# Performance work log

Hardware: AMD Instinct MI355X
Metric: run time of the kernel (lower is better)

## Reference

```python
import jax, jax.numpy as jnp
import numpy as np

PS = 3        # patch_size
RATE = 2      # rate
FS = 3        # fuse_kernel_size
SS = 10.0     # softmax_scale
PAD = (PS - 1) // 2       # tl.calc_padding(ps, 1)
FUSE_PAD = (FS - 1) // 2  # tl.calc_padding(fs, 1)
EPS = 1e-4


def extract_patches(x, ps, stride, pad):
    """x: (B,C,H,W) -> (B, L, C, ps, ps); L row-major over output positions (== F.unfold order)."""
    B, C, H, W = x.shape
    xp = jnp.pad(x, ((0, 0), (0, 0), (pad, pad), (pad, pad)))
    oh = (H + 2 * pad - ps) // stride + 1
    ow = (W + 2 * pad - ps) // stride + 1
    rows = []
    for dy in range(ps):  # small fixed loop (ps=3)
        cols = []
        for dx in range(ps):
            cols.append(xp[:, :, dy:dy + (oh - 1) * stride + 1:stride,
                              dx:dx + (ow - 1) * stride + 1:stride])
        rows.append(jnp.stack(cols, axis=2))           # (B,C,ps,oh,ow)
    p = jnp.stack(rows, axis=2)                        # (B,C,ps,ps,oh,ow)
    return p.reshape(B, C, ps, ps, oh * ow).transpose(0, 4, 1, 2, 3)


def diag_fuse(S, fs, pad):
    """conv2d of (N,N) 'image' with identity fs x fs kernel (diagonal smoothing)."""
    N = S.shape[0]
    Sp = jnp.pad(S, ((pad, pad), (pad, pad)))
    out = Sp[0:N, 0:N]
    for k in range(1, fs):  # fs=3, tiny fixed loop
        out = out + Sp[k:k + N, k:k + N]
    return out


def fuse_scores(S, hr, wr):
    L = hr * wr
    S = diag_fuse(S, FS, FUSE_PAD)
    S = S.reshape(hr, wr, hr, wr).transpose(1, 0, 3, 2).reshape(L, L)
    S = diag_fuse(S, FS, FUSE_PAD)
    S = S.reshape(wr, hr, wr, hr).transpose(1, 0, 3, 2).reshape(L, L)
    return S


def contextual_attention(f_o, b_o, mask_o):
    B, c, h, w = f_o.shape
    # nearest downsample by 1/rate == strided slice
    f = f_o[:, :, ::RATE, ::RATE]
    b = b_o[:, :, ::RATE, ::RATE]
    m = mask_o[:, :, ::RATE, ::RATE]
    hr, wr = f.shape[2], f.shape[3]
    L = hr * wr

    fg = extract_patches(f, PS, 1, PAD)        # (B,L,c,ps,ps) foreground neighborhoods
    bs = extract_patches(b, PS, 1, PAD)        # (B,L,c,ps,ps) shrunk bg patches
    bi = extract_patches(b_o, PS, RATE, PAD)   # (B,L,c,ps,ps) full-res bg patches

    bnorm = jnp.maximum(jnp.sqrt(jnp.sum(bs * bs, axis=(2, 3, 4))), EPS)  # (B,L)
    bsn = bs / bnorm[:, :, None, None, None]

    # score[b,p,q] = <normalized bg patch p, fg neighborhood at position q>
    S = jnp.einsum('bpcij,bqcij->bpq', bsn, fg)  # (B,L,L)
    S = jax.vmap(lambda s: fuse_scores(s, hr, wr))(S)

    # valid-patch indicator from downsampled mask
    mp = extract_patches(m, PS, 1, PAD)                                   # (B,L,1,ps,ps)
    valid = (jnp.mean(mp, axis=(2, 3, 4)) == 0.0).astype(f_o.dtype)       # (B,L)

    score = S.reshape(B, L, hr, wr) * valid[:, :, None, None]
    score = jax.nn.softmax(score * SS, axis=1) * valid[:, :, None, None]

    # conv_transpose2d(score, bi, stride=RATE, padding=PAD, output_padding=1) / 4
    wgt = jnp.flip(bi.transpose(0, 2, 1, 3, 4), axis=(-2, -1))  # (B,c,L,ps,ps)
    pad_cfg = [(PS - 1 - PAD, PS - 1 - PAD + 1)] * 2            # output_padding on high side

    def agg(s, wk):  # s:(L,hr,wr), wk:(c,L,ps,ps)
        return jax.lax.conv_general_dilated(
            s[None], wk, (1, 1), pad_cfg, lhs_dilation=(RATE, RATE),
            dimension_numbers=('NCHW', 'OIHW', 'NCHW'))[0]

    out = jax.vmap(agg)(score, wgt) / 4.0   # (B,c,h,w)
    return out


def setup_inputs() -> dict:
    key = jax.random.key(0)
    k1, k2, k3 = jax.random.split(key, 3)
    f_o = jax.random.normal(k1, (16, 128, 64, 64), dtype=jnp.float32)
    b_o = jax.random.normal(k2, (16, 128, 64, 64), dtype=jnp.float32)
    mask_o = jax.random.randint(k3, (16, 1, 64, 64), 0, 2).astype(jnp.float32)
    return {"f_o": f_o, "b_o": b_o, "mask_o": mask_o}


def reference(f_o, b_o, mask_o):
    return contextual_attention(f_o, b_o, mask_o)
```

## Files before the change

kernel.cpp:

```cpp
#include <hip/hip_runtime.h>
#include <cmath>

#define CC 128
#define HH 64
#define WWI 64
#define LL 1024
#define NB 16
#define MM 1152
#define KC 384
#define TPD 1156

#define SLAB      2977808ul
#define OFF_TP    0
#define OFF_S3T   0
#define OFF_W     0
#define OFF_S2    1336336
#define OFF_SCORET 1336336
#define OFF_POOL  2384912
#define OFF_N2    2974736
#define OFF_BNORM 2975760
#define OFF_VALID 2976784

#define NHROW 132
#define NH1 (NHROW * TPD)
#define NHALO (NH1 + 1024 * NHROW)

typedef __bf16 bf16x8 __attribute__((ext_vector_type(8)));
typedef __bf16 bf16x4 __attribute__((ext_vector_type(4)));
typedef float f32x4 __attribute__((ext_vector_type(4)));

#define GLDS(g, l) __builtin_amdgcn_global_load_lds( \
    (const __attribute__((address_space(1))) unsigned int*)(const void*)(g), \
    (__attribute__((address_space(3))) unsigned int*)(void*)(l), 16, 0, 0)

__global__ __launch_bounds__(256) void k_prep(const float* __restrict__ f_o,
                                              const float* __restrict__ b_o,
                                              float* __restrict__ ws,
                                              int b0) {
    int bz = blockIdx.y, gb = b0 + bz;
    int uy = blockIdx.x;
    __shared__ float lf[128 * 33];
    __shared__ float lb[128 * 33];
    __shared__ float red[8 * 32];
    int tid = threadIdx.x;
    int ux = tid & 31, co = tid >> 5;
    size_t pix = (size_t)(2 * uy) * WWI + 2 * ux;
    const float* fbp = f_o + (size_t)gb * CC * HH * WWI + pix;
    const float* bbp = b_o + (size_t)gb * CC * HH * WWI + pix;
#pragma unroll
    for (int pass = 0; pass < 16; pass++) {
        int c = pass * 8 + co;
        lf[c * 33 + ux] = fbp[(size_t)c * HH * WWI];
        lb[c * 33 + ux] = bbp[(size_t)c * HH * WWI];
    }
    __syncthreads();
    int ux2 = tid >> 3, cg = (tid & 7) * 16;
    int u = uy * 32 + ux2;
    __bf16* bcat = (__bf16*)(ws + (size_t)bz * SLAB + OFF_POOL) + (size_t)u * KC;
    __bf16* fcat = bcat + 393216;
    float s2 = 0.f;
#pragma unroll
    for (int k = 0; k < 16; k++) {
        int c = cg + k;
        float fv = lf[c * 33 + ux2];
        float bv = lb[c * 33 + ux2];
        __bf16 fhi = (__bf16)fv; __bf16 flo = (__bf16)(fv - (float)fhi);
        __bf16 bhi = (__bf16)bv; __bf16 blo = (__bf16)(bv - (float)bhi);
        bcat[c] = bhi; bcat[128 + c] = bhi; bcat[256 + c] = blo;
        fcat[c] = fhi; fcat[128 + c] = flo; fcat[256 + c] = fhi;
        s2 += bv * bv;
    }
    red[(tid & 7) * 32 + ux2] = s2;
    __syncthreads();
    if (tid < 32) {
        float s = 0.f;
#pragma unroll
        for (int k = 0; k < 8; k++) s += red[k * 32 + tid];
        ws[(size_t)bz * SLAB + OFF_N2 + uy * 32 + tid] = s;
    }
}

__global__ __launch_bounds__(256) void k_bnorm_valid(float* __restrict__ ws,
                                                     const float* __restrict__ mask,
                                                     int b0) {
    int t = blockIdx.x * 256 + threadIdx.x;
    int p  = t & (LL - 1);
    int bz = t >> 10;
    int gb = b0 + bz;
    int py = p >> 5, px = p & 31;
    const float* mb = mask + (size_t)gb * HH * WWI;
    const float* n2 = ws + (size_t)bz * SLAB + OFF_N2;
    float s = 0.f, msum = 0.f;
#pragma unroll
    for (int dy = -1; dy <= 1; dy++) {
#pragma unroll
        for (int dx = -1; dx <= 1; dx++) {
            int py2 = py + dy, px2 = px + dx;
            if ((unsigned)py2 < 32u && (unsigned)px2 < 32u) {
                s    += n2[(py2 << 5) | px2];
                msum += mb[(2 * py2) * WWI + 2 * px2];
            }
        }
    }
    ws[(size_t)bz * SLAB + OFF_BNORM + p] = fmaxf(sqrtf(s), 1e-4f);
    ws[(size_t)bz * SLAB + OFF_VALID + p] = (msum == 0.0f) ? 1.0f : 0.0f;
}

__device__ __forceinline__ int halo_idx(int k) {
    if (k < 34) return k;
    if (k < 68) return 1122 + (k - 34);
    if (k < 100) return 34 * (k - 100 + 33);
    return 34 * (k - 132 + 33) + 33;
}

__global__ __launch_bounds__(256) void k_zerohalo(float* __restrict__ ws) {
    int bz = blockIdx.y;
    int t = blockIdx.x * 256 + threadIdx.x;
    if (t >= NHALO) return;
    float* Tp = ws + (size_t)bz * SLAB + OFF_TP;
    if (t < NH1) {
        int R = halo_idx(t / TPD);
        Tp[(size_t)R * TPD + (t % TPD)] = 0.f;
    } else {
        int t2 = t - NH1;
        int ir = t2 / NHROW;
        int R  = 34 * (1 + (ir >> 5)) + 1 + (ir & 31);
        int C  = halo_idx(t2 % NHROW);
        Tp[(size_t)R * TPD + C] = 0.f;
    }
}

template<int KTOT>
__device__ __forceinline__ void gemm_core(const __bf16* __restrict__ Ab,
                                          const __bf16* __restrict__ Bb,
                                          int lda, int ldb, int m0, int n0,
                                          __bf16* As, __bf16* Bs,
                                          f32x4 acc[4][4]) {
    int t = threadIdx.x;
    int lane = t & 63, w = t >> 6;
    int rsub = lane >> 3;
    int g8   = ((lane & 7) ^ (rsub & 7)) * 8;
    int lm = lane & 15, kgf = lane >> 4;
    int wm = (w & 1) * 64, wn = (w >> 1) * 64;

#define ISSUE(kt, buf) do {                                                   \
    int k0_ = (kt) * 64;                                                      \
    _Pragma("unroll")                                                         \
    for (int ci = 0; ci < 4; ci++) {                                          \
        int rb = ci * 32 + w * 8;                                             \
        int r  = rb + rsub;                                                   \
        GLDS(Ab + (size_t)(m0 + r) * lda + k0_ + g8, &As[(buf) + rb * 64]);   \
        GLDS(Bb + (size_t)(n0 + r) * ldb + k0_ + g8, &Bs[(buf) + rb * 64]);   \
    } } while (0)

#define COMPUTE(curoff) do {                                                  \
    _Pragma("unroll")                                                         \
    for (int s2 = 0; s2 < 2; s2++) {                                          \
        bf16x8 af[4], bfr[4];                                                 \
        _Pragma("unroll")                                                     \
        for (int i = 0; i < 4; i++)                                           \
            af[i] = *(const bf16x8*)&As[(curoff) + (wm + i * 16 + lm) * 64 +  \
                                        (((s2 * 4 + kgf) ^ (lm & 7)) * 8)];   \
        _Pragma("unroll")                                                     \
        for (int j = 0; j < 4; j++)                                           \
            bfr[j] = *(const bf16x8*)&Bs[(curoff) + (wn + j * 16 + lm) * 64 + \
                                         (((s2 * 4 + kgf) ^ (lm & 7)) * 8)];  \
        _Pragma("unroll")                                                     \
        for (int i = 0; i < 4; i++)                                           \
            _Pragma("unroll")                                                 \
            for (int j = 0; j < 4; j++)                                       \
                acc[i][j] = __builtin_amdgcn_mfma_f32_16x16x32_bf16(          \
                    af[i], bfr[j], acc[i][j], 0, 0, 0);                       \
    } } while (0)

    const int NIT = KTOT / 64;

    ISSUE(0, 0);
    ISSUE(1, 8192);

#pragma unroll 2
    for (int it = 0; it < NIT - 2; it++) {
        int cur = (it & 1) * 8192;
        asm volatile("s_waitcnt vmcnt(8)" ::: "memory");
        __builtin_amdgcn_sched_barrier(0);
        __builtin_amdgcn_s_barrier();
        COMPUTE(cur);
        __builtin_amdgcn_s_barrier();
        ISSUE(it + 2, cur);
    }
    asm volatile("s_waitcnt vmcnt(8)" ::: "memory");
    __builtin_amdgcn_sched_barrier(0);
    __builtin_amdgcn_s_barrier();
    COMPUTE(((NIT - 2) & 1) * 8192);
    __builtin_amdgcn_s_barrier();
    asm volatile("s_waitcnt vmcnt(0)" ::: "memory");
    __builtin_amdgcn_sched_barrier(0);
    __builtin_amdgcn_s_barrier();
    COMPUTE(((NIT - 1) & 1) * 8192);

#undef ISSUE
#undef COMPUTE
}

__global__ __launch_bounds__(256) void k_gemm_T_mfma(float* __restrict__ ws, int swz) {
    int bz, m0, n0;
    if (swz) {
        bz = blockIdx.x + 8 * (blockIdx.z & 1);
        m0 = blockIdx.y * 128;
        n0 = (blockIdx.z >> 1) * 128;
    } else {
        bz = blockIdx.z; m0 = blockIdx.y * 128; n0 = blockIdx.x * 128;
    }
    const __bf16* Ab = (const __bf16*)(ws + (size_t)bz * SLAB + OFF_POOL);
    const __bf16* Bb = Ab + 393216;
    float* Tp = ws + (size_t)bz * SLAB + OFF_TP;
    __shared__ __align__(16) __bf16 As[2 * 128 * 64];
    __shared__ __align__(16) __bf16 Bs[2 * 128 * 64];
    f32x4 acc[4][4];
#pragma unroll
    for (int i = 0; i < 4; i++)
#pragma unroll
        for (int j = 0; j < 4; j++) acc[i][j] = (f32x4)0.0f;
    gemm_core<KC>(Ab, Bb, KC, KC, m0, n0, As, Bs, acc);
    int lane = threadIdx.x & 63, w = threadIdx.x >> 6;
    int lm = lane & 15, kgf = lane >> 4;
    int wm = (w & 1) * 64, wn = (w >> 1) * 64;
#pragma unroll
    for (int i = 0; i < 4; i++) {
#pragma unroll
        for (int r = 0; r < 4; r++) {
            int m = m0 + wm + i * 16 + kgf * 4 + r;
            float* dst = Tp + (size_t)(((m >> 5) + 1) * 34 + (m & 31) + 1) * TPD;
#pragma unroll
            for (int j = 0; j < 4; j++) {
                int v = n0 + wn + j * 16 + lm;
                dst[((v >> 5) + 1) * 34 + (v & 31) + 1] = acc[i][j][r];
            }
        }
    }
}

__global__ __launch_bounds__(256) void k_s12(float* __restrict__ ws) {
    int bz = blockIdx.y;
    int i0 = blockIdx.x * 8;
    const float* Tp = ws + (size_t)bz * SLAB + OFF_TP;
    const float* bn = ws + (size_t)bz * SLAB + OFF_BNORM;
    float* S2 = ws + (size_t)bz * SLAB + OFF_S2;
    __shared__ float Dsh[10][1024];
    int tid = threadIdx.x;
    for (int rl = 0; rl < 10; rl++) {
        int r = i0 - 1 + rl;
        if ((unsigned)r >= 1024u) continue;
        float invr = 1.0f / bn[r];
        size_t rbase = (size_t)(((r >> 5) + 1) * 34 + (r & 31) + 1) * TPD;
#pragma unroll
        for (int so = 0; so < 4; so++) {
            int s = so * 256 + tid;
            const float* cb = Tp + rbase + ((s >> 5) + 1) * 34 + (s & 31) + 1;
            float d = 0.f;
#pragma unroll
            for (int dy = -1; dy <= 1; dy++)
#pragma unroll
                for (int dx = -1; dx <= 1; dx++)
                    d += cb[dy * (34 * TPD + 34) + dx * (TPD + 1)];
            Dsh[rl][s] = d * invr;
        }
    }
    __syncthreads();
#pragma unroll
    for (int il = 0; il < 8; il++) {
        int i = i0 + il;
        float* orow = S2 + (size_t)i * LL;
#pragma unroll
        for (int jo = 0; jo < 4; jo++) {
            int j = jo * 256 + tid;
            float acc = 0.f;
#pragma unroll
            for (int k1 = -1; k1 <= 1; k1++) {
                int r = i + k1, s = j + k1;
                if ((unsigned)r < 1024u && (unsigned)s < 1024u)
                    acc += Dsh[il + 1 + k1][s];
            }
            orow[j] = acc;
        }
    }
}

__global__ __launch_bounds__(256) void k_st3t(float* __restrict__ ws) {
    int bz = blockIdx.z;
    const float* ib = ws + (size_t)bz * SLAB + OFF_S2;
    float* ob = ws + (size_t)bz * SLAB + OFF_S3T;
    int p0 = blockIdx.y * 64, q0 = blockIdx.x * 64;
    __shared__ float tile[64][65];
    int t = threadIdx.x;
#pragma unroll
    for (int it = 0; it < 16; it++) {
        int e = it * 256 + t;
        int pl = e >> 6, ql = e & 63;
        int p = p0 + pl, q = q0 + ql;
        int sp = ((p & 31) << 5) | (p >> 5);
        int sq = ((q & 31) << 5) | (q >> 5);
        float acc = 0.f;
#pragma unroll
        for (int k = -1; k <= 1; k++) {
            int tp = sp + k, tq = sq + k;
            if ((unsigned)tp < 1024u && (unsigned)tq < 1024u) {
                int row = ((tp & 31) << 5) | (tp >> 5);
                int col = ((tq & 31) << 5) | (tq >> 5);
                acc += ib[(size_t)row * LL + col];
            }
        }
        tile[pl][ql] = acc;
    }
    __syncthreads();
#pragma unroll
    for (int it = 0; it < 16; it++) {
        int e = it * 256 + t;
        int ql = e >> 6, pl = e & 63;
        ob[(size_t)(q0 + ql) * LL + p0 + pl] = tile[pl][ql];
    }
}

__global__ __launch_bounds__(256) void k_softmax_bf(float* __restrict__ ws) {
    int bz = blockIdx.z;
    int lane = threadIdx.x & 63;
    int q = blockIdx.x * 4 + (threadIdx.x >> 6);
    const float* row = ws + (size_t)bz * SLAB + OFF_S3T + (size_t)q * LL;
    const float* vb  = ws + (size_t)bz * SLAB + OFF_VALID;
    __bf16* orow = (__bf16*)(ws + (size_t)bz * SLAB + OFF_SCORET) + (size_t)q * LL;

    float4 v[4], vl[4];
#pragma unroll
    for (int i = 0; i < 4; i++) {
        int p = lane * 4 + i * 256;
        float4 s = *(const float4*)(row + p);
        float4 m = *(const float4*)(vb + p);
        v[i] = {s.x * m.x, s.y * m.y, s.z * m.z, s.w * m.w};
        vl[i] = m;
    }
    float mx = -1e30f;
#pragma unroll
    for (int i = 0; i < 4; i++)
        mx = fmaxf(mx, fmaxf(fmaxf(v[i].x, v[i].y), fmaxf(v[i].z, v[i].w)));
#pragma unroll
    for (int k = 1; k < 64; k <<= 1)
        mx = fmaxf(mx, __shfl_xor(mx, k, 64));
    float sum = 0.f;
    float4 e[4];
#pragma unroll
    for (int i = 0; i < 4; i++) {
        e[i].x = __expf(10.f * (v[i].x - mx));
        e[i].y = __expf(10.f * (v[i].y - mx));
        e[i].z = __expf(10.f * (v[i].z - mx));
        e[i].w = __expf(10.f * (v[i].w - mx));
        sum += e[i].x + e[i].y + e[i].z + e[i].w;
    }
#pragma unroll
    for (int k = 1; k < 64; k <<= 1)
        sum += __shfl_xor(sum, k, 64);
    float inv = 1.0f / sum;
#pragma unroll
    for (int i = 0; i < 4; i++) {
        bf16x4 o;
        o[0] = (__bf16)(e[i].x * inv * vl[i].x);
        o[1] = (__bf16)(e[i].y * inv * vl[i].y);
        o[2] = (__bf16)(e[i].z * inv * vl[i].z);
        o[3] = (__bf16)(e[i].w * inv * vl[i].w);
        *(bf16x4*)(orow + lane * 4 + i * 256) = o;
    }
}

__global__ __launch_bounds__(256) void k_makeA(const float* __restrict__ b_o,
                                               float* __restrict__ ws,
                                               int b0) {
    int c = blockIdx.x, bz = blockIdx.y, gb = b0 + bz;
    __shared__ float img[64][65];
    int t = threadIdx.x;
    const float4* src = (const float4*)(b_o + (size_t)(gb * CC + c) * HH * WWI);
#pragma unroll
    for (int it = 0; it < 4; it++) {
        int idx = it * 256 + t;
        float4 v = src[idx];
        int row = idx >> 4, col4 = (idx & 15) * 4;
        img[row][col4] = v.x; img[row][col4 + 1] = v.y;
        img[row][col4 + 2] = v.z; img[row][col4 + 3] = v.w;
    }
    __syncthreads();
    __bf16* Ab = (__bf16*)(ws + (size_t)bz * SLAB + OFF_POOL) + (size_t)c * 9 * LL;
    int py = t >> 3, px4 = (t & 7) * 4;
#pragma unroll
    for (int jy = 0; jy < 3; jy++) {
        int row = 2 * py + jy - 1;
        bool rok = (unsigned)row < 64u;
#pragma unroll
        for (int jx = 0; jx < 3; jx++) {
            bf16x4 o;
#pragma unroll
            for (int e = 0; e < 4; e++) {
                int col = 2 * (px4 + e) + jx - 1;
                float v = (rok && (unsigned)col < 64u) ? img[rok ? row : 0][(unsigned)col < 64u ? col : 0] : 0.f;
                o[e] = (__bf16)v;
            }
            *(bf16x4*)(Ab + (size_t)(jy * 3 + jx) * LL + t * 4) = o;
        }
    }
}

__global__ __launch_bounds__(256) void k_gemm_W_mfma(float* __restrict__ ws, int swz) {
    int bz, m0, n0;
    if (swz) {
        bz = blockIdx.x + 8 * (blockIdx.z & 1);
        m0 = blockIdx.y * 128;
        n0 = (blockIdx.z >> 1) * 128;
    } else {
        bz = blockIdx.z; m0 = blockIdx.y * 128; n0 = blockIdx.x * 128;
    }
    const __bf16* Ab = (const __bf16*)(ws + (size_t)bz * SLAB + OFF_POOL);
    const __bf16* Bb = (const __bf16*)(ws + (size_t)bz * SLAB + OFF_SCORET);
    __bf16* Wb = (__bf16*)(ws + (size_t)bz * SLAB + OFF_W);
    __shared__ __align__(16) __bf16 As[2 * 128 * 64];
    __shared__ __align__(16) __bf16 Bs[2 * 128 * 64];
    f32x4 acc[4][4];
#pragma unroll
    for (int i = 0; i < 4; i++)
#pragma unroll
        for (int j = 0; j < 4; j++) acc[i][j] = (f32x4)0.0f;
    gemm_core<LL>(Ab, Bb, LL, LL, m0, n0, As, Bs, acc);
    int lane = threadIdx.x & 63, w = threadIdx.x >> 6;
    int lm = lane & 15, kgf = lane >> 4;
    int wm = (w & 1) * 64, wn = (w >> 1) * 64;
#pragma unroll
    for (int i = 0; i < 4; i++) {
#pragma unroll
        for (int r = 0; r < 4; r++) {
            int m = m0 + wm + i * 16 + kgf * 4 + r;
            __bf16* dst = Wb + (size_t)m * LL + n0 + wn + lm;
#pragma unroll
            for (int j = 0; j < 4; j++)
                dst[j * 16] = (__bf16)acc[i][j][r];
        }
    }
}

__global__ __launch_bounds__(256) void k_gather(const float* __restrict__ ws,
                                                float* __restrict__ outp,
                                                int b0) {
    int t = blockIdx.x * 256 + threadIdx.x;
    int ox = t & 63, oy = (t >> 6) & 63, c = (t >> 12) & 127, bz = t >> 19;
    const __bf16* Wb = (const __bf16*)(ws + (size_t)bz * SLAB + OFF_W);
    int qyA = (oy + 1) >> 1;
    int jyA = (oy & 1) ? 0 : 1;
    int vA  = (qyA < 32);
    int qyB = (oy - 1) >> 1;
    int vB  = (oy & 1);
    int qxA = (ox + 1) >> 1;
    int jxA = (ox & 1) ? 0 : 1;
    int uA  = (qxA < 32);
    int qxB = (ox - 1) >> 1;
    int uB  = (ox & 1);
    const __bf16* base = Wb + (size_t)c * 9 * LL;
    float s = 0.f;
    if (vA && uA) s += (float)base[(size_t)(jyA * 3 + jxA) * LL + qyA * 32 + qxA];
    if (vA && uB) s += (float)base[(size_t)(jyA * 3 + 2)   * LL + qyA * 32 + qxB];
    if (vB && uA) s += (float)base[(size_t)(2 * 3 + jxA)   * LL + qyB * 32 + qxA];
    if (vB && uB) s += (float)base[(size_t)(2 * 3 + 2)     * LL + qyB * 32 + qxB];
    outp[((size_t)((b0 + bz) * CC + c) * HH + oy) * WWI + ox] = 0.25f * s;
}

extern "C" void kernel_launch(void* const* d_in, const int* in_sizes, int n_in,
                              void* d_out, int out_size, void* d_ws, size_t ws_size,
                              hipStream_t stream) {
    (void)in_sizes; (void)n_in; (void)out_size;
    const float* f_o  = (const float*)d_in[0];
    const float* b_o  = (const float*)d_in[1];
    const float* mask = (const float*)d_in[2];
    float* out = (float*)d_out;

    int G = (int)(ws_size / (SLAB * sizeof(float)));
    if (G < 1) G = 1;
    if (G > NB) G = NB;
    float* ws = (float*)d_ws;

    for (int b0 = 0; b0 < NB; b0 += G) {
        int Gc = NB - b0 < G ? NB - b0 : G;
        int swz = (Gc == 16) ? 1 : 0;
        k_prep<<<dim3(32, Gc), 256, 0, stream>>>(f_o, b_o, ws, b0);
        k_bnorm_valid<<<dim3(Gc * 4), 256, 0, stream>>>(ws, mask, b0);
        k_zerohalo<<<dim3((NHALO + 255) / 256, Gc), 256, 0, stream>>>(ws);
        k_gemm_T_mfma<<<dim3(8, 8, Gc), 256, 0, stream>>>(ws, swz);
        k_s12<<<dim3(128, Gc), 256, 0, stream>>>(ws);
        k_st3t<<<dim3(16, 16, Gc), 256, 0, stream>>>(ws);
        k_softmax_bf<<<dim3(256, 1, Gc), 256, 0, stream>>>(ws);
        k_makeA<<<dim3(CC, Gc), 256, 0, stream>>>(b_o, ws, b0);
        k_gemm_W_mfma<<<dim3(8, 9, Gc), 256, 0, stream>>>(ws, swz);
        k_gather<<<dim3(Gc * 2048), 256, 0, stream>>>(ws, out, b0);
    }
}
```

Measured before the change: 360.7 us.

## Add 256x256-tile 512-thread W GEMM with interleaved prefetch and XCD-aware block mapping

Adds a new GEMM kernel for the W product that uses 256x256 output tiles with 8 waves, XOR-swizzled LDS, double-buffered global-to-LDS loads interleaved with MFMA groups, and s_setprio around MFMA bursts. Blocks are remapped so consecutive logical tiles land on the same XCD, improving L2 reuse. It is used only when all 16 batches fit in the workspace, otherwise the old 128x128 kernel runs. Larger tiles cut redundant operand loads but raise register/LDS pressure (128KB LDS) and waste work on the clamped tail rows beyond 1152.

```diff
diff --git a/kernel.cpp b/kernel.cpp
--- a/kernel.cpp
+++ b/kernel.cpp
@@ -240,6 +240,162 @@
     }
 }
 
+__global__ __launch_bounds__(512, 2) void k_gemm_W256(float* __restrict__ ws) {
+    int d = blockIdx.x;
+    int logical = (d & 7) * 40 + (d >> 3);
+    int bz  = logical / 20;
+    int t20 = logical % 20;
+    int m0 = (t20 >> 2) * 256;
+    int n0 = (t20 & 3) * 256;
+    const __bf16* Ab = (const __bf16*)(ws + (size_t)bz * SLAB + OFF_POOL);
+    const __bf16* Bb = (const __bf16*)(ws + (size_t)bz * SLAB + OFF_SCORET);
+    __bf16* Wb = (__bf16*)(ws + (size_t)bz * SLAB + OFF_W);
+    __shared__ __align__(16) __bf16 As[2 * 256 * 64];
+    __shared__ __align__(16) __bf16 Bs[2 * 256 * 64];
+
+    int t = threadIdx.x;
+    int lane = t & 63, w = t >> 6;
+    int rsub = lane >> 3;
+    int g8   = ((lane & 7) ^ (rsub & 7)) * 8;
+    int lm = lane & 15, kgf = lane >> 4;
+    int wr = (w >> 2) * 128;
+    int wc = (w & 3) * 64;
+
+    f32x4 acc[8][4];
+#pragma unroll
+    for (int i = 0; i < 8; i++)
+#pragma unroll
+        for (int j = 0; j < 4; j++) acc[i][j] = (f32x4)0.0f;
+
+#define WSTAGE(ci, nb, k1_) do {                                              \
+    int rb = (ci) * 64 + w * 8;                                               \
+    int rA = m0 + rb + rsub; if (rA > MM - 1) rA = MM - 1;                    \
+    GLDS(Ab + (size_t)rA * LL + (k1_) + g8, &As[(nb) + rb * 64]);             \
+    GLDS(Bb + (size_t)(n0 + rb + rsub) * LL + (k1_) + g8, &Bs[(nb) + rb * 64]); \
+    } while (0)
+
+#define RD_A(mh, bo) do {                                                     \
+    _Pragma("unroll")                                                         \
+    for (int mi = 0; mi < 4; mi++)                                            \
+        _Pragma("unroll")                                                     \
+        for (int ks = 0; ks < 2; ks++)                                        \
+            af[mi][ks] = *(const bf16x8*)&As[(bo) +                           \
+                (wr + (mh) * 64 + mi * 16 + lm) * 64 +                        \
+                (((ks * 4 + kgf) ^ (lm & 7)) * 8)];                           \
+    } while (0)
+
+#define RD_B(njlo, bo) do {                                                   \
+    _Pragma("unroll")                                                         \
+    for (int nj = 0; nj < 2; nj++)                                            \
+        _Pragma("unroll")                                                     \
+        for (int ks = 0; ks < 2; ks++)                                        \
+            bfr[(njlo) + nj][ks] = *(const bf16x8*)&Bs[(bo) +                 \
+                (wc + ((njlo) + nj) * 16 + lm) * 64 +                         \
+                (((ks * 4 + kgf) ^ (lm & 7)) * 8)];                           \
+    } while (0)
+
+#define QMFMA(mb, njlo) do {                                                  \
+    __builtin_amdgcn_s_setprio(1);                                            \
+    _Pragma("unroll")                                                         \
+    for (int ks = 0; ks < 2; ks++)                                            \
+        _Pragma("unroll")                                                     \
+        for (int mi = 0; mi < 4; mi++)                                        \
+            _Pragma("unroll")                                                 \
+            for (int nj = 0; nj < 2; nj++)                                    \
+                acc[(mb) + mi][(njlo) + nj] =                                 \
+                    __builtin_amdgcn_mfma_f32_16x16x32_bf16(                  \
+                        af[mi][ks], bfr[(njlo) + nj][ks],                     \
+                        acc[(mb) + mi][(njlo) + nj], 0, 0, 0);                \
+    __builtin_amdgcn_s_setprio(0);                                            \
+    } while (0)
+
+#pragma unroll
+    for (int ci = 0; ci < 4; ci++) WSTAGE(ci, 0, 0);
+    asm volatile("s_waitcnt vmcnt(0)" ::: "memory");
+    __builtin_amdgcn_sched_barrier(0);
+    __builtin_amdgcn_s_barrier();
+
+#pragma unroll 2
+    for (int kt = 0; kt < 16; kt++) {
+        int bo = (kt & 1) * 16384;
+        int nb = bo ^ 16384;
+        int k1 = (kt + 1) * 64;
+        bool pf = (kt < 15);
+        bf16x8 af[4][2], bfr[4][2];
+        RD_A(0, bo);
+        RD_B(0, bo);
+        if (pf) WSTAGE(0, nb, k1);
+        QMFMA(0, 0);
+        RD_B(2, bo);
+        if (pf) { WSTAGE(1, nb, k1); WSTAGE(2, nb, k1); }
+        QMFMA(0, 2);
+        RD_A(1, bo);
+        if (pf) WSTAGE(3, nb, k1);
+        QMFMA(4, 2);
+        QMFMA(4, 0);
+        if (pf) {
+            asm volatile("s_waitcnt vmcnt(0)" ::: "memory");
+            __builtin_amdgcn_sched_barrier(0);
+            __builtin_amdgcn_s_barrier();
+        }
+    }
+
+#undef WSTAGE
+#undef RD_A
+#undef RD_B
+#undef QMFMA
+
+#pragma unroll
+    for (int mf = 0; mf < 8; mf++) {
+#pragma unroll
+        for (int r = 0; r < 4; r++) {
+            int m = m0 + wr + mf * 16 + kgf * 4 + r;
+            if (m < MM) {
+                __bf16* dst = Wb + (size_t)m * LL + n0 + wc + lm;
+#pragma unroll
+                for (int nj = 0; nj < 4; nj++)
+                    dst[nj * 16] = (__bf16)acc[mf][nj][r];
+            }
+        }
+    }
+}
+
+__global__ __launch_bounds__(256) void k_gemm_W_mfma(float* __restrict__ ws, int swz) {
+    int bz, m0, n0;
+    if (swz) {
+        bz = blockIdx.x + 8 * (blockIdx.z & 1);
+        m0 = blockIdx.y * 128;
+        n0 = (blockIdx.z >> 1) * 128;
+    } else {
+        bz = blockIdx.z; m0 = blockIdx.y * 128; n0 = blockIdx.x * 128;
+    }
+    const __bf16* Ab = (const __bf16*)(ws + (size_t)bz * SLAB + OFF_POOL);
+    const __bf16* Bb = (const __bf16*)(ws + (size_t)bz * SLAB + OFF_SCORET);
+    __bf16* Wb = (__bf16*)(ws + (size_t)bz * SLAB + OFF_W);
+    __shared__ __align__(16) __bf16 As[2 * 128 * 64];
+    __shared__ __align__(16) __bf16 Bs[2 * 128 * 64];
+    f32x4 acc[4][4];
+#pragma unroll
+    for (int i = 0; i < 4; i++)
+#pragma unroll
+        for (int j = 0; j < 4; j++) acc[i][j] = (f32x4)0.0f;
+    gemm_core<LL>(Ab, Bb, LL, LL, m0, n0, As, Bs, acc);
+    int lane = threadIdx.x & 63, w = threadIdx.x >> 6;
+    int lm = lane & 15, kgf = lane >> 4;
+    int wm = (w & 1) * 64, wn = (w >> 1) * 64;
+#pragma unroll
+    for (int i = 0; i < 4; i++) {
+#pragma unroll
+        for (int r = 0; r < 4; r++) {
+            int m = m0 + wm + i * 16 + kgf * 4 + r;
+            __bf16* dst = Wb + (size_t)m * LL + n0 + wn + lm;
+#pragma unroll
+            for (int j = 0; j < 4; j++)
+                dst[j * 16] = (__bf16)acc[i][j][r];
+        }
+    }
+}
+
 __global__ __launch_bounds__(256) void k_s12(float* __restrict__ ws) {
     int bz = blockIdx.y;
     int i0 = blockIdx.x * 8;
@@ -402,42 +558,6 @@
                 o[e] = (__bf16)v;
             }
             *(bf16x4*)(Ab + (size_t)(jy * 3 + jx) * LL + t * 4) = o;
-        }
-    }
-}
-
-__global__ __launch_bounds__(256) void k_gemm_W_mfma(float* __restrict__ ws, int swz) {
-    int bz, m0, n0;
-    if (swz) {
-        bz = blockIdx.x + 8 * (blockIdx.z & 1);
-        m0 = blockIdx.y * 128;
-        n0 = (blockIdx.z >> 1) * 128;
-    } else {
-        bz = blockIdx.z; m0 = blockIdx.y * 128; n0 = blockIdx.x * 128;
-    }
-    const __bf16* Ab = (const __bf16*)(ws + (size_t)bz * SLAB + OFF_POOL);
-    const __bf16* Bb = (const __bf16*)(ws + (size_t)bz * SLAB + OFF_SCORET);
-    __bf16* Wb = (__bf16*)(ws + (size_t)bz * SLAB + OFF_W);
-    __shared__ __align__(16) __bf16 As[2 * 128 * 64];
-    __shared__ __align__(16) __bf16 Bs[2 * 128 * 64];
-    f32x4 acc[4][4];
-#pragma unroll
-    for (int i = 0; i < 4; i++)
-#pragma unroll
-        for (int j = 0; j < 4; j++) acc[i][j] = (f32x4)0.0f;
-    gemm_core<LL>(Ab, Bb, LL, LL, m0, n0, As, Bs, acc);
-    int lane = threadIdx.x & 63, w = threadIdx.x >> 6;
-    int lm = lane & 15, kgf = lane >> 4;
-    int wm = (w & 1) * 64, wn = (w >> 1) * 64;
-#pragma unroll
-    for (int i = 0; i < 4; i++) {
-#pragma unroll
-        for (int r = 0; r < 4; r++) {
-            int m = m0 + wm + i * 16 + kgf * 4 + r;
-            __bf16* dst = Wb + (size_t)m * LL + n0 + wn + lm;
-#pragma unroll
-            for (int j = 0; j < 4; j++)
-                dst[j * 16] = (__bf16)acc[i][j][r];
         }
     }
 }
@@ -492,7 +612,11 @@
         k_st3t<<<dim3(16, 16, Gc), 256, 0, stream>>>(ws);
         k_softmax_bf<<<dim3(256, 1, Gc), 256, 0, stream>>>(ws);
         k_makeA<<<dim3(CC, Gc), 256, 0, stream>>>(b_o, ws, b0);
-        k_gemm_W_mfma<<<dim3(8, 9, Gc), 256, 0, stream>>>(ws, swz);
+        if (Gc == NB) {
+            k_gemm_W256<<<dim3(320), 512, 0, stream>>>(ws);
+        } else {
+            k_gemm_W_mfma<<<dim3(8, 9, Gc), 256, 0, stream>>>(ws, swz);
+        }
         k_gather<<<dim3(Gc * 2048), 256, 0, stream>>>(ws, out, b0);
     }
 }
```

Measured after the change: 359.5 us. About the same (-0.3%).
